# Kernel tuning notes

Hardware: AMD Instinct MI355X
Metric: run time of the kernel (lower is better)

## Reference

```python
import jax, jax.numpy as jnp
import numpy as np

EPS = 1e-5
HEADS = 8
SR = 4


def bn(x, gamma, beta, mean, var):
    # BatchNorm in inference form; channel axis = 1
    shape = (1, -1) + (1,) * (x.ndim - 2)
    inv = gamma.reshape(shape) / jnp.sqrt(var.reshape(shape) + EPS)
    return (x - mean.reshape(shape)) * inv + beta.reshape(shape)


def setup_inputs() -> dict:
    key = jax.random.key(0)
    ks = jax.random.split(key, 8)
    B, C, H, W = 2, 256, 128, 128
    N = H * W
    conv1d_std = np.sqrt(2.0 / C)            # fan_out = 1*C
    conv2d_std = np.sqrt(2.0 / (SR * SR * C))  # fan_out = sr*sr*C
    return {
        "x": jax.random.normal(ks[0], (B, C, N), dtype=jnp.float32),
        "w_q": jax.random.normal(ks[1], (C, C), dtype=jnp.float32) * conv1d_std,
        "w_k": jax.random.normal(ks[2], (C, C), dtype=jnp.float32) * conv1d_std,
        "w_sr": jax.random.normal(ks[3], (C, C, SR, SR), dtype=jnp.float32) * conv2d_std,
        "sr_gamma": jnp.ones((C,), jnp.float32),
        "sr_beta": jnp.zeros((C,), jnp.float32),
        "sr_mean": jnp.zeros((C,), jnp.float32),
        "sr_var": jnp.ones((C,), jnp.float32),
        "w_proj": jax.random.normal(ks[4], (C, C), dtype=jnp.float32) * conv1d_std,
        "proj_gamma": jnp.ones((C,), jnp.float32),
        "proj_beta": jnp.zeros((C,), jnp.float32),
        "proj_mean": jnp.zeros((C,), jnp.float32),
        "proj_var": jnp.ones((C,), jnp.float32),
        "H": 128,
        "W": 128,
    }


def reference(x, w_q, w_k, w_sr, sr_gamma, sr_beta, sr_mean, sr_var,
              w_proj, proj_gamma, proj_beta, proj_mean, proj_var, H, W):
    B, C, N = x.shape
    hd = C // HEADS
    scale = hd ** -0.5
    # q: Conv1d(k=1) == channel matmul -> (B, heads, N, hd)
    q = jnp.einsum('oc,bcn->bon', w_q, x).reshape(B, HEADS, hd, N).transpose(0, 1, 3, 2)
    # spatial reduction: Conv2d(k=SR, s=SR) as patch-reshape + einsum, then BN
    xp = x.reshape(B, C, H // SR, SR, W // SR, SR)
    xr = jnp.einsum('bchpwq,ocpq->bohw', xp, w_sr).reshape(B, C, (H // SR) * (W // SR))
    xr = bn(xr, sr_gamma, sr_beta, sr_mean, sr_var)
    # k: (B, heads, hd, N_kv)
    k = jnp.einsum('oc,bcm->bom', w_k, xr).reshape(B, HEADS, hd, -1)
    # scores (B, heads, N, N_kv) -> max over kv
    scores = jnp.einsum('bhnd,bhdm->bhnm', q, k) * scale
    attn = scores.max(axis=-1)                # (B, heads, N)
    # v = mean-pooled x, identical per head -> matmul collapses to sum over heads
    v = x.mean(axis=-1)                       # (B, C)
    out = jnp.einsum('bhn,bc->bcn', attn, v)  # (B, C, N)
    out = jnp.einsum('oc,bcn->bon', w_proj, out)
    return bn(out, proj_gamma, proj_beta, proj_mean, proj_var)
```

## Files before the change

kernel.cpp:

```cpp
#include <hip/hip_runtime.h>
#include <hip/hip_bf16.h>
#include <math.h>

#define EPSF 1e-5f
#define SCALE 0.17677669529663687f

typedef __bf16 bf16x8 __attribute__((ext_vector_type(8)));
typedef __bf16 bf16x4 __attribute__((ext_vector_type(4)));
typedef float f32x4 __attribute__((ext_vector_type(4)));


__global__ __launch_bounds__(256) void k_ab(const float* __restrict__ v,
                                            const float* __restrict__ wproj,
                                            const float* __restrict__ pg,
                                            const float* __restrict__ pb,
                                            const float* __restrict__ pm,
                                            const float* __restrict__ pvar,
                                            float* __restrict__ A,
                                            float* __restrict__ B0) {
    __shared__ float vl[256];
    int t = threadIdx.x, b = blockIdx.x;
    vl[t] = v[b * 256 + t] * (1.0f / 16384.0f);
    __syncthreads();
    const float* wr = wproj + t * 256;
    float s = 0.f;
#pragma unroll 8
    for (int c = 0; c < 256; c += 4) {
        float4 w = *(const float4*)&wr[c];
        s += w.x * vl[c] + w.y * vl[c + 1] + w.z * vl[c + 2] + w.w * vl[c + 3];
    }
    float inv = pg[t] / sqrtf(pvar[t] + EPSF);
    A[b * 256 + t] = s * inv;
    if (b == 0) B0[t] = pb[t] - pm[t] * inv;
}

__global__ __launch_bounds__(256) void k_wprep(const float* __restrict__ wq,
                                               const float* __restrict__ wk,
                                               const float* __restrict__ wsr,
                                               __bf16* __restrict__ wqf,
                                               __bf16* __restrict__ wkb,
                                               __bf16* __restrict__ wsrf,
                                               float* __restrict__ v) {
    int bi = blockIdx.x, t = threadIdx.x;
    if (bi < 32) {
        if (bi == 0) { v[t] = 0.f; v[256 + t] = 0.f; }
        int tt = bi * 256 + t;
        int o = tt >> 5, chunk = tt & 31;
        float4 v0 = *(const float4*)&wq[o * 256 + (chunk << 3)];
        float4 v1 = *(const float4*)&wq[o * 256 + (chunk << 3) + 4];
        bf16x8 p;
        p[0] = (__bf16)v0.x; p[1] = (__bf16)v0.y; p[2] = (__bf16)v0.z; p[3] = (__bf16)v0.w;
        p[4] = (__bf16)v1.x; p[5] = (__bf16)v1.y; p[6] = (__bf16)v1.z; p[7] = (__bf16)v1.w;
        int cc = chunk >> 2, quad = chunk & 3;
        *(bf16x8*)&wqf[(((((o >> 4) << 3) + cc) << 6) + (quad << 4) + (o & 15)) << 3] = p;
    } else if (bi < 64) {
        int e = (bi - 32) * 256 + t;
        float4 v0 = *(const float4*)&wk[e << 3];
        float4 v1 = *(const float4*)&wk[(e << 3) + 4];
        bf16x8 p;
        p[0] = (__bf16)(v0.x * SCALE); p[1] = (__bf16)(v0.y * SCALE);
        p[2] = (__bf16)(v0.z * SCALE); p[3] = (__bf16)(v0.w * SCALE);
        p[4] = (__bf16)(v1.x * SCALE); p[5] = (__bf16)(v1.y * SCALE);
        p[6] = (__bf16)(v1.z * SCALE); p[7] = (__bf16)(v1.w * SCALE);
        *(bf16x8*)&wkb[e << 3] = p;
    } else {
        int tt = (bi - 64) * 256 + t;
        int o = tt >> 9, chunk = tt & 511;
        float4 v0 = *(const float4*)&wsr[o * 4096 + (chunk << 3)];
        float4 v1 = *(const float4*)&wsr[o * 4096 + (chunk << 3) + 4];
        bf16x8 p;
        p[0] = (__bf16)v0.x; p[1] = (__bf16)v0.y; p[2] = (__bf16)v0.z; p[3] = (__bf16)v0.w;
        p[4] = (__bf16)v1.x; p[5] = (__bf16)v1.y; p[6] = (__bf16)v1.z; p[7] = (__bf16)v1.w;
        int cc = chunk >> 2, quad = chunk & 3;
        *(bf16x8*)&wsrf[(((((o >> 4) << 7) + cc) << 6) + (quad << 4) + (o & 15)) << 3] = p;
    }
}

__global__ __launch_bounds__(256) void k_im2col(const float* __restrict__ x,
                                                __bf16* __restrict__ Pbf,
                                                float* __restrict__ v) {
    __shared__ float csum[64];
    int t = threadIdx.x, bid = blockIdx.x;
    int b = bid >> 7, hm = (bid >> 2) & 31, ccg = bid & 3;
    int wm = t >> 3, c8 = t & 7;
    if (t < 64) csum[t] = 0.f;
    __syncthreads();
    const int mtile = (hm << 1) + (wm >> 4);
    const int ln = wm & 15;
#pragma unroll 2
    for (int cci = 0; cci < 8; ++cci) {
        int c = (ccg << 6) + (cci << 3) + c8;
        const float* src = x + ((size_t)(b * 256 + c) << 14) + (hm << 9) + (wm << 2);
        bf16x8 o0, o1;
        float s = 0.f;
#pragma unroll
        for (int p = 0; p < 2; ++p) {
            float4 vv = *(const float4*)&src[p << 7];
            s += vv.x + vv.y + vv.z + vv.w;
            o0[p * 4 + 0] = (__bf16)vv.x; o0[p * 4 + 1] = (__bf16)vv.y;
            o0[p * 4 + 2] = (__bf16)vv.z; o0[p * 4 + 3] = (__bf16)vv.w;
        }
#pragma unroll
        for (int p = 0; p < 2; ++p) {
            float4 vv = *(const float4*)&src[(p + 2) << 7];
            s += vv.x + vv.y + vv.z + vv.w;
            o1[p * 4 + 0] = (__bf16)vv.x; o1[p * 4 + 1] = (__bf16)vv.y;
            o1[p * 4 + 2] = (__bf16)vv.z; o1[p * 4 + 3] = (__bf16)vv.w;
        }
        size_t d0 = (((((size_t)(b * 64 + mtile) << 7) + (c >> 1)) << 6) +
                     (((c & 1) << 1) << 4) + ln) << 3;
        *(bf16x8*)&Pbf[d0] = o0;
        *(bf16x8*)&Pbf[d0 + 128] = o1;
        atomicAdd(&csum[(cci << 3) + c8], s);
    }
    __syncthreads();
    if (t < 64) atomicAdd(&v[b * 256 + (ccg << 6) + t], csum[t]);
}

__global__ __launch_bounds__(256) void k_conv1(const __bf16* __restrict__ Pbf,
                                               const __bf16* __restrict__ wsrf,
                                               float* __restrict__ xrp) {
    const int t = threadIdx.x, bid = blockIdx.x;
    const int b = bid & 1, mt = (bid >> 1) & 31, ks = bid >> 6;
    const int w = t >> 6, lane = t & 63, ln = lane & 15, quad = lane >> 4;
    f32x4 acc[2][4];
#pragma unroll
    for (int nt = 0; nt < 2; ++nt)
#pragma unroll
        for (int ot = 0; ot < 4; ++ot) acc[nt][ot] = (f32x4){0.f, 0.f, 0.f, 0.f};
    const __bf16* pa = Pbf + (((((size_t)(b * 64 + mt * 2)) << 7) + (ks << 5)) << 9) + (lane << 3);
    const __bf16* pbm = wsrf + ((((size_t)(w << 2) << 7) + (ks << 5)) << 9) + (lane << 3);
#pragma unroll 4
    for (int cci = 0; cci < 32; ++cci) {
        const int cb = cci << 9;
        bf16x8 af[2], bfr[4];
#pragma unroll
        for (int nt = 0; nt < 2; ++nt) af[nt] = *(const bf16x8*)&pa[(nt << 16) + cb];
#pragma unroll
        for (int ot = 0; ot < 4; ++ot) bfr[ot] = *(const bf16x8*)&pbm[(ot << 16) + cb];
#pragma unroll
        for (int nt = 0; nt < 2; ++nt)
#pragma unroll
            for (int ot = 0; ot < 4; ++ot)
                acc[nt][ot] = __builtin_amdgcn_mfma_f32_16x16x32_bf16(af[nt], bfr[ot],
                                                                     acc[nt][ot], 0, 0, 0);
    }
    float* dst = xrp + (((size_t)((ks << 1) + b) << 10) << 8);
#pragma unroll
    for (int nt = 0; nt < 2; ++nt)
#pragma unroll
        for (int ot = 0; ot < 4; ++ot)
#pragma unroll
            for (int r = 0; r < 4; ++r) {
                int m = (mt << 5) + (nt << 4) + (quad << 2) + r;
                int o = (w << 6) + (ot << 4) + ln;
                dst[m * 256 + o] = acc[nt][ot][r];
            }
}

__global__ __launch_bounds__(256) void k_comb2(const float* __restrict__ xrp,
                                               const float* __restrict__ sg,
                                               const float* __restrict__ sb,
                                               const float* __restrict__ smn,
                                               const float* __restrict__ svar,
                                               __bf16* __restrict__ xrb) {
    int t = threadIdx.x, bid = blockIdx.x;
    int b = bid >> 8, m = ((bid & 255) << 2) + (t >> 6);
    int o4 = (t & 63) << 2;
    size_t base = (((size_t)b << 10) + m) << 8;
    float4 s0 = *(const float4*)&xrp[base + o4];
    float4 s1 = *(const float4*)&xrp[524288 + base + o4];
    float4 s2 = *(const float4*)&xrp[1048576 + base + o4];
    float4 s3 = *(const float4*)&xrp[1572864 + base + o4];
    float4 g = *(const float4*)&sg[o4];
    float4 vr = *(const float4*)&svar[o4];
    float4 mn = *(const float4*)&smn[o4];
    float4 bt = *(const float4*)&sb[o4];
    bf16x4 r;
    r[0] = (__bf16)((s0.x + s1.x + s2.x + s3.x - mn.x) * (g.x / sqrtf(vr.x + EPSF)) + bt.x);
    r[1] = (__bf16)((s0.y + s1.y + s2.y + s3.y - mn.y) * (g.y / sqrtf(vr.y + EPSF)) + bt.y);
    r[2] = (__bf16)((s0.z + s1.z + s2.z + s3.z - mn.z) * (g.z / sqrtf(vr.z + EPSF)) + bt.z);
    r[3] = (__bf16)((s0.w + s1.w + s2.w + s3.w - mn.w) * (g.w / sqrtf(vr.w + EPSF)) + bt.w);
    *(bf16x4*)&xrb[base + o4] = r;
}

__global__ __launch_bounds__(256) void k_kmat2(const __bf16* __restrict__ xrb,
                                               const __bf16* __restrict__ wkb,
                                               __bf16* __restrict__ kkbh) {
    const int t = threadIdx.x, bid = blockIdx.x;
    const int b = bid >> 4, mt = bid & 15;
    const int w = t >> 6, lane = t & 63, ln = lane & 15, quad = lane >> 4;
    f32x4 acc[4][4];
#pragma unroll
    for (int nt = 0; nt < 4; ++nt)
#pragma unroll
        for (int ot = 0; ot < 4; ++ot) acc[nt][ot] = (f32x4){0.f, 0.f, 0.f, 0.f};
    const __bf16* pa = xrb + ((((size_t)b << 10) + (mt << 6) + ln) << 8) + (quad << 3);
    const __bf16* pbm = wkb + (((w << 6) + ln) << 8) + (quad << 3);
#pragma unroll 2
    for (int cc = 0; cc < 8; ++cc) {
        const int cb = cc << 5;
        bf16x8 af[4], bfr[4];
#pragma unroll
        for (int nt = 0; nt < 4; ++nt) af[nt] = *(const bf16x8*)&pa[(nt << 12) + cb];
#pragma unroll
        for (int ot = 0; ot < 4; ++ot) bfr[ot] = *(const bf16x8*)&pbm[(ot << 12) + cb];
#pragma unroll
        for (int nt = 0; nt < 4; ++nt)
#pragma unroll
            for (int ot = 0; ot < 4; ++ot)
                acc[nt][ot] = __builtin_amdgcn_mfma_f32_16x16x32_bf16(af[nt], bfr[ot],
                                                                     acc[nt][ot], 0, 0, 0);
    }
#pragma unroll
    for (int nt = 0; nt < 4; ++nt)
#pragma unroll
        for (int ot = 0; ot < 4; ++ot)
#pragma unroll
            for (int r = 0; r < 4; ++r) {
                int m = (mt << 6) + (nt << 4) + (quad << 2) + r;
                int h = (w << 1) + (ot >> 1);
                int d = ((ot & 1) << 4) + ln;
                kkbh[(((size_t)(b * 8 + h)) << 15) + (m << 5) + d] = (__bf16)acc[nt][ot][r];
            }
}

__global__ __launch_bounds__(256) void k_xt(const float* __restrict__ x,
                                            __bf16* __restrict__ xTf) {
    __shared__ float ts[32 * 132];
    int t = threadIdx.x, bid = blockIdx.x;
    int b = bid >> 7, n0 = (bid & 127) << 7;
    const int n = n0 + (t >> 1);
    const int ntile = n >> 4, ln = n & 15;
    const int ch = (t & 1) << 4;
    for (int s8 = 0; s8 < 8; ++s8) {
        int c0 = s8 << 5;
        __syncthreads();
#pragma unroll
        for (int i = 0; i < 4; ++i) {
            int e = t + (i << 8);
            int c = e >> 5, n4 = (e & 31) << 2;
            *(float4*)&ts[c * 132 + n4] =
                *(const float4*)&x[((size_t)(b * 256 + c0 + c) << 14) + n0 + n4];
        }
        __syncthreads();
        int nl = t >> 1;
        bf16x8 p0, p1;
#pragma unroll
        for (int j = 0; j < 8; ++j) p0[j] = (__bf16)ts[(ch + j) * 132 + nl];
#pragma unroll
        for (int j = 0; j < 8; ++j) p1[j] = (__bf16)ts[(ch + 8 + j) * 132 + nl];
        int q0 = ch >> 3;
        size_t base = ((((size_t)(b * 1024 + ntile) << 3) + s8) << 6);
        *(bf16x8*)&xTf[(base + (q0 << 4) + ln) << 3] = p0;
        *(bf16x8*)&xTf[(base + ((q0 + 1) << 4) + ln) << 3] = p1;
    }
}

__global__ __launch_bounds__(256) void k_scores2(const __bf16* __restrict__ xTf,
                                                 const __bf16* __restrict__ wqf,
                                                 const __bf16* __restrict__ kkbh,
                                                 const float* __restrict__ A,
                                                 const float* __restrict__ B0,
                                                 float* __restrict__ out) {
    __shared__ __align__(16) __bf16 qs[64 * 264];
    __shared__ float smax[256];
    __shared__ float ss[64];
    __shared__ float sA[256], sB[256];
    const int t = threadIdx.x;
    const int w = t >> 6;
    const int lane = t & 63;
    const int ln = lane & 15;
    const int quad = lane >> 4;
    const int b = blockIdx.x >> 8;
    const int n0 = (blockIdx.x & 255) << 6;
    if (t < 64) ss[t] = 0.f;

    f32x4 acc[4][4];
#pragma unroll
    for (int nt = 0; nt < 4; ++nt)
#pragma unroll
        for (int ot = 0; ot < 4; ++ot) acc[nt][ot] = (f32x4){0.f, 0.f, 0.f, 0.f};
    const __bf16* pa = xTf + (((size_t)(b * 1024 + (n0 >> 4))) << 12) + (lane << 3);
    const __bf16* pbm = wqf + ((size_t)w << 14) + (lane << 3);
#pragma unroll 2
    for (int cc = 0; cc < 8; ++cc) {
        const int cb = cc << 9;
        bf16x8 af[4], bfr[4];
#pragma unroll
        for (int nt = 0; nt < 4; ++nt) af[nt] = *(const bf16x8*)&pa[(nt << 12) + cb];
#pragma unroll
        for (int ot = 0; ot < 4; ++ot) bfr[ot] = *(const bf16x8*)&pbm[(ot << 12) + cb];
#pragma unroll
        for (int nt = 0; nt < 4; ++nt)
#pragma unroll
            for (int ot = 0; ot < 4; ++ot)
                acc[nt][ot] = __builtin_amdgcn_mfma_f32_16x16x32_bf16(af[nt], bfr[ot],
                                                                      acc[nt][ot], 0, 0, 0);
    }
#pragma unroll
    for (int nt = 0; nt < 4; ++nt)
#pragma unroll
        for (int ot = 0; ot < 4; ++ot)
#pragma unroll
            for (int r = 0; r < 4; ++r)
                qs[((nt << 4) + (quad << 2) + r) * 264 + (w << 6) + (ot << 4) + ln] =
                    (__bf16)acc[nt][ot][r];
    __syncthreads();

    const f32x4 zf = {0.f, 0.f, 0.f, 0.f};
    for (int h = 0; h < 8; ++h) {
        bf16x8 qb[4];
#pragma unroll
        for (int nt = 0; nt < 4; ++nt)
            qb[nt] = *(const bf16x8*)&qs[((nt << 4) + ln) * 264 + (h << 5) + (quad << 3)];
        float rmx[4] = {-INFINITY, -INFINITY, -INFINITY, -INFINITY};
        const __bf16* kb_base = kkbh + ((size_t)(b * 8 + h) << 15) + (ln << 5) + (quad << 3);
#pragma unroll 4
        for (int i = 0; i < 16; ++i) {
            bf16x8 kb = *(const bf16x8*)&kb_base[((w << 8) + (i << 4)) << 5];
#pragma unroll
            for (int nt = 0; nt < 4; ++nt) {
                f32x4 d = __builtin_amdgcn_mfma_f32_16x16x32_bf16(kb, qb[nt], zf, 0, 0, 0);
                rmx[nt] = fmaxf(rmx[nt], fmaxf(fmaxf(d[0], d[1]), fmaxf(d[2], d[3])));
            }
        }
#pragma unroll
        for (int nt = 0; nt < 4; ++nt) {
            rmx[nt] = fmaxf(rmx[nt], __shfl_xor(rmx[nt], 16, 64));
            rmx[nt] = fmaxf(rmx[nt], __shfl_xor(rmx[nt], 32, 64));
        }
        if (lane < 16) {
#pragma unroll
            for (int nt = 0; nt < 4; ++nt) smax[(w << 6) + (nt << 4) + lane] = rmx[nt];
        }
        __syncthreads();
        if (t < 64) {
            float vv = fmaxf(fmaxf(smax[t], smax[64 + t]), fmaxf(smax[128 + t], smax[192 + t]));
            ss[t] += vv;
        }
        __syncthreads();
    }

    sA[t] = A[b * 256 + t];
    sB[t] = B0[t];
    __syncthreads();
#pragma unroll
    for (int i = 0; i < 16; ++i) {
        int e = t + (i << 8);
        int c = e >> 4, n4 = (e & 15) << 2;
        float4 s4 = *(const float4*)&ss[n4];
        float a = sA[c], bb = sB[c];
        float4 o4 = make_float4(fmaf(a, s4.x, bb), fmaf(a, s4.y, bb),
                                fmaf(a, s4.z, bb), fmaf(a, s4.w, bb));
        *(float4*)&out[((size_t)(b * 256 + c) << 14) + n0 + n4] = o4;
    }
}

extern "C" void kernel_launch(void* const* d_in, const int* in_sizes, int n_in,
                              void* d_out, int out_size, void* d_ws, size_t ws_size,
                              hipStream_t stream) {
    const float* x    = (const float*)d_in[0];
    const float* wq   = (const float*)d_in[1];
    const float* wk   = (const float*)d_in[2];
    const float* wsr  = (const float*)d_in[3];
    const float* sg   = (const float*)d_in[4];
    const float* sb   = (const float*)d_in[5];
    const float* smn  = (const float*)d_in[6];
    const float* svr  = (const float*)d_in[7];
    const float* wproj= (const float*)d_in[8];
    const float* pg   = (const float*)d_in[9];
    const float* pb   = (const float*)d_in[10];
    const float* pm   = (const float*)d_in[11];
    const float* pvr  = (const float*)d_in[12];
    float* out = (float*)d_out;

    char* W = (char*)d_ws;
    float*  w_v   = (float*) (W + 0);
    float*  w_A   = (float*) (W + 4096);
    float*  w_B0  = (float*) (W + 8192);
    __bf16* w_wqf = (__bf16*)(W + 16384);
    __bf16* w_wkb = (__bf16*)(W + 147456);
    __bf16* w_wsrf= (__bf16*)(W + 278528);
    __bf16* w_xrb = (__bf16*)(W + 2375680);
    __bf16* w_kkbh= (__bf16*)(W + 2899968);
    float*  w_xrp = (float*) (W + 3948544);
    __bf16* w_Pbf = (__bf16*)(W + 12337152);
    __bf16* w_xTf = (__bf16*)(W + 12337152);

    k_wprep<<<576, 256, 0, stream>>>(wq, wk, wsr, w_wqf, w_wkb, w_wsrf, w_v);
    k_im2col<<<256, 256, 0, stream>>>(x, w_Pbf, w_v);
    k_ab<<<2, 256, 0, stream>>>(w_v, wproj, pg, pb, pm, pvr, w_A, w_B0);
    k_conv1<<<256, 256, 0, stream>>>(w_Pbf, w_wsrf, w_xrp);
    k_comb2<<<512, 256, 0, stream>>>(w_xrp, sg, sb, smn, svr, w_xrb);
    k_kmat2<<<32, 256, 0, stream>>>(w_xrb, w_wkb, w_kkbh);
    k_xt<<<256, 256, 0, stream>>>(x, w_xTf);
    k_scores2<<<512, 256, 0, stream>>>(w_xTf, w_wqf, w_kkbh, w_A, w_B0, out);
}
```

Baseline: 208.8 us.

## Split conv, kmat, im2col and transpose kernels into more blocks; batch score maxima

Doubles or quadruples the grid sizes of im2col, the strided conv GEMM, the K projection and the x transpose by giving each block a smaller tile, so more of the GPU's compute units get work. In the scores kernel all 16 K fragments are preloaded into registers per head, and the per-head barrier pair is replaced by one reduction after the head loop, using a larger shared max buffer. The cost is less operand reuse per block, more global reads of the weight fragments, and higher register and LDS pressure in the scores kernel, which may lower occupancy.

```diff
diff --git a/kernel.cpp b/kernel.cpp
--- a/kernel.cpp
+++ b/kernel.cpp
@@ -79,17 +79,17 @@
 __global__ __launch_bounds__(256) void k_im2col(const float* __restrict__ x,
                                                 __bf16* __restrict__ Pbf,
                                                 float* __restrict__ v) {
-    __shared__ float csum[64];
+    __shared__ float csum[32];
     int t = threadIdx.x, bid = blockIdx.x;
-    int b = bid >> 7, hm = (bid >> 2) & 31, ccg = bid & 3;
+    int b = bid >> 8, hm = (bid >> 3) & 31, ccg = bid & 7;
     int wm = t >> 3, c8 = t & 7;
-    if (t < 64) csum[t] = 0.f;
+    if (t < 32) csum[t] = 0.f;
     __syncthreads();
     const int mtile = (hm << 1) + (wm >> 4);
     const int ln = wm & 15;
-#pragma unroll 2
-    for (int cci = 0; cci < 8; ++cci) {
-        int c = (ccg << 6) + (cci << 3) + c8;
+#pragma unroll
+    for (int cci = 0; cci < 4; ++cci) {
+        int c = (ccg << 5) + (cci << 3) + c8;
         const float* src = x + ((size_t)(b * 256 + c) << 14) + (hm << 9) + (wm << 2);
         bf16x8 o0, o1;
         float s = 0.f;
@@ -114,48 +114,40 @@
         atomicAdd(&csum[(cci << 3) + c8], s);
     }
     __syncthreads();
-    if (t < 64) atomicAdd(&v[b * 256 + (ccg << 6) + t], csum[t]);
+    if (t < 32) atomicAdd(&v[b * 256 + (ccg << 5) + t], csum[t]);
 }
 
 __global__ __launch_bounds__(256) void k_conv1(const __bf16* __restrict__ Pbf,
                                                const __bf16* __restrict__ wsrf,
                                                float* __restrict__ xrp) {
     const int t = threadIdx.x, bid = blockIdx.x;
-    const int b = bid & 1, mt = (bid >> 1) & 31, ks = bid >> 6;
+    const int b = bid & 1, mt = (bid >> 1) & 63, ks = bid >> 7;
     const int w = t >> 6, lane = t & 63, ln = lane & 15, quad = lane >> 4;
-    f32x4 acc[2][4];
-#pragma unroll
-    for (int nt = 0; nt < 2; ++nt)
-#pragma unroll
-        for (int ot = 0; ot < 4; ++ot) acc[nt][ot] = (f32x4){0.f, 0.f, 0.f, 0.f};
-    const __bf16* pa = Pbf + (((((size_t)(b * 64 + mt * 2)) << 7) + (ks << 5)) << 9) + (lane << 3);
+    f32x4 acc[4];
+#pragma unroll
+    for (int ot = 0; ot < 4; ++ot) acc[ot] = (f32x4){0.f, 0.f, 0.f, 0.f};
+    const __bf16* pa = Pbf + ((((size_t)(b * 64 + mt) << 7) + (ks << 5)) << 9) + (lane << 3);
     const __bf16* pbm = wsrf + ((((size_t)(w << 2) << 7) + (ks << 5)) << 9) + (lane << 3);
 #pragma unroll 4
     for (int cci = 0; cci < 32; ++cci) {
         const int cb = cci << 9;
-        bf16x8 af[2], bfr[4];
-#pragma unroll
-        for (int nt = 0; nt < 2; ++nt) af[nt] = *(const bf16x8*)&pa[(nt << 16) + cb];
+        bf16x8 af = *(const bf16x8*)&pa[cb];
+        bf16x8 bfr[4];
 #pragma unroll
         for (int ot = 0; ot < 4; ++ot) bfr[ot] = *(const bf16x8*)&pbm[(ot << 16) + cb];
 #pragma unroll
-        for (int nt = 0; nt < 2; ++nt)
-#pragma unroll
-            for (int ot = 0; ot < 4; ++ot)
-                acc[nt][ot] = __builtin_amdgcn_mfma_f32_16x16x32_bf16(af[nt], bfr[ot],
-                                                                     acc[nt][ot], 0, 0, 0);
-    }
-    float* dst = xrp + (((size_t)((ks << 1) + b) << 10) << 8);
-#pragma unroll
-    for (int nt = 0; nt < 2; ++nt)
-#pragma unroll
         for (int ot = 0; ot < 4; ++ot)
-#pragma unroll
-            for (int r = 0; r < 4; ++r) {
-                int m = (mt << 5) + (nt << 4) + (quad << 2) + r;
-                int o = (w << 6) + (ot << 4) + ln;
-                dst[m * 256 + o] = acc[nt][ot][r];
-            }
+            acc[ot] = __builtin_amdgcn_mfma_f32_16x16x32_bf16(af, bfr[ot], acc[ot], 0, 0, 0);
+    }
+    float* dst = xrp + ((size_t)((ks << 1) + b) << 18);
+#pragma unroll
+    for (int ot = 0; ot < 4; ++ot)
+#pragma unroll
+        for (int r = 0; r < 4; ++r) {
+            int m = (mt << 4) + (quad << 2) + r;
+            int o = (w << 6) + (ot << 4) + ln;
+            dst[m * 256 + o] = acc[ot][r];
+        }
 }
 
 __global__ __launch_bounds__(256) void k_comb2(const float* __restrict__ xrp,
@@ -188,72 +180,60 @@
                                                const __bf16* __restrict__ wkb,
                                                __bf16* __restrict__ kkbh) {
     const int t = threadIdx.x, bid = blockIdx.x;
-    const int b = bid >> 4, mt = bid & 15;
+    const int b = bid >> 6, mt = bid & 63;
     const int w = t >> 6, lane = t & 63, ln = lane & 15, quad = lane >> 4;
-    f32x4 acc[4][4];
-#pragma unroll
-    for (int nt = 0; nt < 4; ++nt)
-#pragma unroll
-        for (int ot = 0; ot < 4; ++ot) acc[nt][ot] = (f32x4){0.f, 0.f, 0.f, 0.f};
-    const __bf16* pa = xrb + ((((size_t)b << 10) + (mt << 6) + ln) << 8) + (quad << 3);
+    f32x4 acc[4];
+#pragma unroll
+    for (int ot = 0; ot < 4; ++ot) acc[ot] = (f32x4){0.f, 0.f, 0.f, 0.f};
+    const __bf16* pa = xrb + ((((size_t)b << 10) + (mt << 4) + ln) << 8) + (quad << 3);
     const __bf16* pbm = wkb + (((w << 6) + ln) << 8) + (quad << 3);
-#pragma unroll 2
+#pragma unroll
     for (int cc = 0; cc < 8; ++cc) {
         const int cb = cc << 5;
-        bf16x8 af[4], bfr[4];
-#pragma unroll
-        for (int nt = 0; nt < 4; ++nt) af[nt] = *(const bf16x8*)&pa[(nt << 12) + cb];
+        bf16x8 af = *(const bf16x8*)&pa[cb];
+        bf16x8 bfr[4];
 #pragma unroll
         for (int ot = 0; ot < 4; ++ot) bfr[ot] = *(const bf16x8*)&pbm[(ot << 12) + cb];
 #pragma unroll
-        for (int nt = 0; nt < 4; ++nt)
-#pragma unroll
-            for (int ot = 0; ot < 4; ++ot)
-                acc[nt][ot] = __builtin_amdgcn_mfma_f32_16x16x32_bf16(af[nt], bfr[ot],
-                                                                     acc[nt][ot], 0, 0, 0);
-    }
-#pragma unroll
-    for (int nt = 0; nt < 4; ++nt)
-#pragma unroll
         for (int ot = 0; ot < 4; ++ot)
-#pragma unroll
-            for (int r = 0; r < 4; ++r) {
-                int m = (mt << 6) + (nt << 4) + (quad << 2) + r;
-                int h = (w << 1) + (ot >> 1);
-                int d = ((ot & 1) << 4) + ln;
-                kkbh[(((size_t)(b * 8 + h)) << 15) + (m << 5) + d] = (__bf16)acc[nt][ot][r];
-            }
+            acc[ot] = __builtin_amdgcn_mfma_f32_16x16x32_bf16(af, bfr[ot], acc[ot], 0, 0, 0);
+    }
+#pragma unroll
+    for (int ot = 0; ot < 4; ++ot)
+#pragma unroll
+        for (int r = 0; r < 4; ++r) {
+            int m = (mt << 4) + (quad << 2) + r;
+            int h = (w << 1) + (ot >> 1);
+            int d = ((ot & 1) << 4) + ln;
+            kkbh[(((size_t)(b * 8 + h)) << 15) + (m << 5) + d] = (__bf16)acc[ot][r];
+        }
 }
 
 __global__ __launch_bounds__(256) void k_xt(const float* __restrict__ x,
                                             __bf16* __restrict__ xTf) {
-    __shared__ float ts[32 * 132];
+    __shared__ float ts[32 * 68];
     int t = threadIdx.x, bid = blockIdx.x;
-    int b = bid >> 7, n0 = (bid & 127) << 7;
-    const int n = n0 + (t >> 1);
-    const int ntile = n >> 4, ln = n & 15;
-    const int ch = (t & 1) << 4;
+    int b = bid >> 8, n0 = (bid & 255) << 6;
+    const int nl = t >> 2;
+    const int ch = (t & 3) << 3;
+    const int n = n0 + nl;
+    const int ntile = n >> 4, ln = n & 15, quad = ch >> 3;
+    const int cl = t >> 3;
+    const int n8 = (t & 7) << 3;
     for (int s8 = 0; s8 < 8; ++s8) {
         int c0 = s8 << 5;
         __syncthreads();
-#pragma unroll
-        for (int i = 0; i < 4; ++i) {
-            int e = t + (i << 8);
-            int c = e >> 5, n4 = (e & 31) << 2;
-            *(float4*)&ts[c * 132 + n4] =
-                *(const float4*)&x[((size_t)(b * 256 + c0 + c) << 14) + n0 + n4];
+        {
+            const float* src = &x[((size_t)(b * 256 + c0 + cl) << 14) + n0 + n8];
+            *(float4*)&ts[cl * 68 + n8] = *(const float4*)&src[0];
+            *(float4*)&ts[cl * 68 + n8 + 4] = *(const float4*)&src[4];
         }
         __syncthreads();
-        int nl = t >> 1;
-        bf16x8 p0, p1;
-#pragma unroll
-        for (int j = 0; j < 8; ++j) p0[j] = (__bf16)ts[(ch + j) * 132 + nl];
-#pragma unroll
-        for (int j = 0; j < 8; ++j) p1[j] = (__bf16)ts[(ch + 8 + j) * 132 + nl];
-        int q0 = ch >> 3;
-        size_t base = ((((size_t)(b * 1024 + ntile) << 3) + s8) << 6);
-        *(bf16x8*)&xTf[(base + (q0 << 4) + ln) << 3] = p0;
-        *(bf16x8*)&xTf[(base + ((q0 + 1) << 4) + ln) << 3] = p1;
+        bf16x8 p;
+#pragma unroll
+        for (int j = 0; j < 8; ++j) p[j] = (__bf16)ts[(ch + j) * 68 + nl];
+        *(bf16x8*)&xTf[(((((size_t)(b * 1024 + ntile) << 3) + s8) << 6) +
+                        (quad << 4) + ln) << 3] = p;
     }
 }
 
@@ -264,7 +244,7 @@
                                                  const float* __restrict__ B0,
                                                  float* __restrict__ out) {
     __shared__ __align__(16) __bf16 qs[64 * 264];
-    __shared__ float smax[256];
+    __shared__ float smax[2048];
     __shared__ float ss[64];
     __shared__ float sA[256], sB[256];
     const int t = threadIdx.x;
@@ -274,7 +254,6 @@
     const int quad = lane >> 4;
     const int b = blockIdx.x >> 8;
     const int n0 = (blockIdx.x & 255) << 6;
-    if (t < 64) ss[t] = 0.f;
 
     f32x4 acc[4][4];
 #pragma unroll
@@ -314,17 +293,19 @@
 #pragma unroll
         for (int nt = 0; nt < 4; ++nt)
             qb[nt] = *(const bf16x8*)&qs[((nt << 4) + ln) * 264 + (h << 5) + (quad << 3)];
+        const __bf16* kb_base = kkbh + ((size_t)(b * 8 + h) << 15) + (ln << 5) + (quad << 3);
+        bf16x8 kb[16];
+#pragma unroll
+        for (int i = 0; i < 16; ++i)
+            kb[i] = *(const bf16x8*)&kb_base[((w << 8) + (i << 4)) << 5];
         float rmx[4] = {-INFINITY, -INFINITY, -INFINITY, -INFINITY};
-        const __bf16* kb_base = kkbh + ((size_t)(b * 8 + h) << 15) + (ln << 5) + (quad << 3);
-#pragma unroll 4
-        for (int i = 0; i < 16; ++i) {
-            bf16x8 kb = *(const bf16x8*)&kb_base[((w << 8) + (i << 4)) << 5];
+#pragma unroll
+        for (int i = 0; i < 16; ++i)
 #pragma unroll
             for (int nt = 0; nt < 4; ++nt) {
-                f32x4 d = __builtin_amdgcn_mfma_f32_16x16x32_bf16(kb, qb[nt], zf, 0, 0, 0);
+                f32x4 d = __builtin_amdgcn_mfma_f32_16x16x32_bf16(kb[i], qb[nt], zf, 0, 0, 0);
                 rmx[nt] = fmaxf(rmx[nt], fmaxf(fmaxf(d[0], d[1]), fmaxf(d[2], d[3])));
             }
-        }
 #pragma unroll
         for (int nt = 0; nt < 4; ++nt) {
             rmx[nt] = fmaxf(rmx[nt], __shfl_xor(rmx[nt], 16, 64));
@@ -332,19 +313,25 @@
         }
         if (lane < 16) {
 #pragma unroll
-            for (int nt = 0; nt < 4; ++nt) smax[(w << 6) + (nt << 4) + lane] = rmx[nt];
-        }
-        __syncthreads();
-        if (t < 64) {
-            float vv = fmaxf(fmaxf(smax[t], smax[64 + t]), fmaxf(smax[128 + t], smax[192 + t]));
-            ss[t] += vv;
-        }
-        __syncthreads();
-    }
-
+            for (int nt = 0; nt < 4; ++nt)
+                smax[(w << 9) + (h << 6) + (nt << 4) + lane] = rmx[nt];
+        }
+    }
+    __syncthreads();
+    if (t < 64) {
+        float ssum = 0.f;
+#pragma unroll
+        for (int h = 0; h < 8; ++h) {
+            float vv = fmaxf(fmaxf(smax[(h << 6) + t], smax[512 + (h << 6) + t]),
+                             fmaxf(smax[1024 + (h << 6) + t], smax[1536 + (h << 6) + t]));
+            ssum += vv;
+        }
+        ss[t] = ssum;
+    }
     sA[t] = A[b * 256 + t];
     sB[t] = B0[t];
     __syncthreads();
+
 #pragma unroll
     for (int i = 0; i < 16; ++i) {
         int e = t + (i << 8);
@@ -389,11 +376,11 @@
     __bf16* w_xTf = (__bf16*)(W + 12337152);
 
     k_wprep<<<576, 256, 0, stream>>>(wq, wk, wsr, w_wqf, w_wkb, w_wsrf, w_v);
-    k_im2col<<<256, 256, 0, stream>>>(x, w_Pbf, w_v);
+    k_im2col<<<512, 256, 0, stream>>>(x, w_Pbf, w_v);
     k_ab<<<2, 256, 0, stream>>>(w_v, wproj, pg, pb, pm, pvr, w_A, w_B0);
-    k_conv1<<<256, 256, 0, stream>>>(w_Pbf, w_wsrf, w_xrp);
+    k_conv1<<<512, 256, 0, stream>>>(w_Pbf, w_wsrf, w_xrp);
     k_comb2<<<512, 256, 0, stream>>>(w_xrp, sg, sb, smn, svr, w_xrb);
-    k_kmat2<<<32, 256, 0, stream>>>(w_xrb, w_wkb, w_kkbh);
-    k_xt<<<256, 256, 0, stream>>>(x, w_xTf);
+    k_kmat2<<<128, 256, 0, stream>>>(w_xrb, w_wkb, w_kkbh);
+    k_xt<<<512, 256, 0, stream>>>(x, w_xTf);
     k_scores2<<<512, 256, 0, stream>>>(w_xTf, w_wqf, w_kkbh, w_A, w_B0, out);
 }
```

Result: faster. 194.8 us (-6.7%).
